# Optimization experiments

Measured on AMD Instinct MI355X. Metric: run time of the kernel, lower is better.

The kernel has to match this reference:

```python
import jax, jax.numpy as jnp
import numpy as np

D_MODEL = 64; D_INNER = 64; D_STATE = 8; DT_RANK = 4; D_CONV = 4
B, C, H, W = 16, 1024, 32, 32


def _silu(x):
    return x * jax.nn.sigmoid(x)


def _layernorm(x, g, b, eps=1e-5):
    m = x.mean(-1, keepdims=True)
    v = ((x - m) ** 2).mean(-1, keepdims=True)
    return (x - m) * jax.lax.rsqrt(v + eps) * g + b


def _rmsnorm(x, w, eps=1e-5):
    return x * jax.lax.rsqrt((x * x).mean(-1, keepdims=True) + eps) * w


def _causal_conv1d(x, w, b):
    # x: [B, D, L]; depthwise causal conv, kernel w: [D, K]
    D = x.shape[1]; K = w.shape[1]
    xp = jnp.pad(x, ((0, 0), (0, 0), (K - 1, 0)))
    y = jax.lax.conv_general_dilated(xp, w[:, None, :], (1,), 'VALID',
                                     dimension_numbers=('NCH', 'OIH', 'NCH'),
                                     feature_group_count=D)
    return y + b[None, :, None]


def _selective_scan(x, z, A_log, Dvec, xproj_w, dt_w, dt_b):
    # x, z: [B, D, L]
    A = -jnp.exp(A_log)                                    # [D, N]
    xdb = jnp.einsum('bdl,kd->blk', x, xproj_w)            # [B, L, R+2N]
    dt_lr = xdb[..., :DT_RANK]
    Bc = xdb[..., DT_RANK:DT_RANK + D_STATE]               # [B, L, N]
    Cc = xdb[..., DT_RANK + D_STATE:]                      # [B, L, N]
    dt = jax.nn.softplus(jnp.einsum('blr,dr->bld', dt_lr, dt_w) + dt_b)  # [B, L, D]
    dA = jnp.exp(dt[..., None] * A[None, None])            # [B, L, D, N]
    dBx = dt[..., None] * Bc[:, :, None, :] * x.transpose(0, 2, 1)[..., None]  # [B, L, D, N]

    def step(h, inp):
        dA_t, dBx_t, C_t = inp
        h = dA_t * h + dBx_t                               # [B, D, N]
        return h, jnp.einsum('bdn,bn->bd', h, C_t)

    h0 = jnp.zeros((x.shape[0], x.shape[1], D_STATE), x.dtype)
    _, ys = jax.lax.scan(step, h0, (dA.transpose(1, 0, 2, 3),
                                    dBx.transpose(1, 0, 2, 3),
                                    Cc.transpose(1, 0, 2)))
    y = ys.transpose(1, 2, 0) + Dvec[None, :, None] * x    # [B, D, L]
    return y * _silu(z)


def _mamba_branch(u, in_w, conv_w, conv_b, xproj_w, dt_w, dt_b, A_log, Dvec):
    # u: [B, L, d_model]
    xz = jnp.einsum('bld,ed->bel', u, in_w)                # [B, 2*D_INNER, L]
    x, z = jnp.split(xz, 2, axis=1)
    x = _silu(_causal_conv1d(x, conv_w, conv_b))
    return _selective_scan(x, z, A_log, Dvec, xproj_w, dt_w, dt_b)


def setup_inputs():
    key = jax.random.key(0)
    ks = jax.random.split(key, 20)
    rn = lambda i, shape, s=1.0: jax.random.normal(ks[i], shape, dtype=jnp.float32) * s
    s4d = jnp.log(jnp.tile(jnp.arange(1, D_STATE + 1, dtype=jnp.float32)[None, :], (D_INNER, 1)))
    return {
        'img1': rn(0, (B, C, H, W)),
        'img2': rn(1, (B, C, H, W)),
        'pre_w': rn(2, (D_MODEL, 1), 0.3),
        'pre_b': rn(3, (D_MODEL,), 0.1),
        'ln_g': jnp.ones((D_MODEL,), jnp.float32),
        'ln_b': jnp.zeros((D_MODEL,), jnp.float32),
        'in_w': rn(4, (2 * D_INNER, D_MODEL), 0.1),
        'in_b_w': rn(5, (2 * D_INNER, D_MODEL), 0.1),
        'conv_w': rn(6, (D_INNER, D_CONV), 0.3),
        'conv_bias': rn(7, (D_INNER,), 0.1),
        'convb_w': rn(8, (D_INNER, D_CONV), 0.3),
        'convb_bias': rn(9, (D_INNER,), 0.1),
        'xproj_w': rn(10, (DT_RANK + 2 * D_STATE, D_INNER), 0.1),
        'xprojb_w': rn(11, (DT_RANK + 2 * D_STATE, D_INNER), 0.1),
        'dt_w': rn(12, (D_INNER, DT_RANK), 0.1),
        'dt_bias': rn(13, (D_INNER,), 0.1),
        'dtb_w': rn(14, (D_INNER, DT_RANK), 0.1),
        'dtb_bias': rn(15, (D_INNER,), 0.1),
        'A_log': s4d,
        'A_b_log': s4d,
        'Dp': jnp.ones((D_INNER,), jnp.float32),
        'Dp_b': jnp.ones((D_INNER,), jnp.float32),
        'norm_w': jnp.ones((D_INNER,), jnp.float32),
        'out_w': rn(16, (D_MODEL, D_INNER), 0.1),
        'post_w': rn(17, (1, D_MODEL), 0.3),
        'post_b': jnp.zeros((1,), jnp.float32),
    }


def reference(img1, img2, pre_w, pre_b, ln_g, ln_b, in_w, in_b_w, conv_w, conv_bias,
              convb_w, convb_bias, xproj_w, xprojb_w, dt_w, dt_bias, dtb_w, dtb_bias,
              A_log, A_b_log, Dp, Dp_b, norm_w, out_w, post_w, post_b):
    # AdaptiveMaxPool2d((1,1)) + squeeze(-1) -> [B, C, 1]
    p1 = jnp.max(img1, axis=(2, 3))[..., None]
    p2 = jnp.max(img2, axis=(2, 3))[..., None]
    # pre_linear: Linear(1, 64) then LayerNorm(64)  -> [B, C(=L), 64]
    x1 = _layernorm(p1 * pre_w[:, 0] + pre_b, ln_g, ln_b)
    x2 = _layernorm(p2 * pre_w[:, 0] + pre_b, ln_g, ln_b)
    # bimamba v3 (cross): forward scan on x1, reversed scan on extra_emb=x2
    out_f = _mamba_branch(x1, in_w, conv_w, conv_bias, xproj_w, dt_w, dt_bias, A_log, Dp)
    out_b = _mamba_branch(x2[:, ::-1, :], in_b_w, convb_w, convb_bias, xprojb_w,
                          dtb_w, dtb_bias, A_b_log, Dp_b)[:, :, ::-1]
    y = (out_f + out_b).transpose(0, 2, 1)                 # [B, L, D_INNER]
    y = _rmsnorm(y, norm_w)                                # use_norm=True
    y = jnp.einsum('bld,ed->ble', y, out_w)                # out_proj (no bias)
    att = jnp.einsum('bld,od->blo', y, post_w) + post_b    # post_linear -> [B, C, 1]
    return jax.nn.sigmoid(att[..., None])                  # [B, C, 1, 1]
```

## Files before the change

### kernel.cpp

```cpp
#include <hip/hip_runtime.h>
#include <math.h>

typedef float    f32x4 __attribute__((ext_vector_type(4)));
typedef _Float16 f16x4 __attribute__((ext_vector_type(4)));

#define NCH 32
#define CLN 32

#define OFF_P     0
#define OFF_Q     524288
#define OFF_HIN   1048576
#define OFF_AN    1572864
#define OFF_WZ    1638400
#define OFF_VEW   1638784
#define OFF_AL2   1638848
#define OFF_TILEH 1640448
#define DTT_H 0
#define SXT_H 2097152
#define BCT_H 4194304

#define LOG2E 1.4426950408889634f
#define LN2   0.6931471805599453f

__device__ __forceinline__ float fexp2(float x){ return __builtin_amdgcn_exp2f(x); }
__device__ __forceinline__ float flog2(float x){ return __builtin_amdgcn_logf(x); }
__device__ __forceinline__ float frcp (float x){ return __builtin_amdgcn_rcpf(x); }
__device__ __forceinline__ float fsigmoid(float x){ return frcp(1.f + fexp2(-x*LOG2E)); }
__device__ __forceinline__ float fsilu(float x){ return x * fsigmoid(x); }
__device__ __forceinline__ float fsoftplus(float x){
  return fmaxf(x, 0.f) + LN2 * flog2(1.f + fexp2(-fabsf(x)*LOG2E));
}

__device__ __forceinline__ float wave_rsum(float v){
  #pragma unroll
  for (int o = 1; o < 64; o <<= 1) v += __shfl_xor(v, o, 64);
  return v;
}
__device__ __forceinline__ float wave_rmax(float v){
  #pragma unroll
  for (int o = 1; o < 64; o <<= 1) v = fmaxf(v, __shfl_xor(v, o, 64));
  return v;
}

struct Smem {
  float a1[36], a2[36], a3[36];
  float xpt[20*65];
  float dtlr[32*4];
  float sxt[64*37];
  float dtt[32*64];
  float bct[32*16];
  float gw[64], gb[64], lnbs[64];
  float W[384];
  float cst[4];
};

__device__ __forceinline__ void consts_ln(float* gw, float* gb, float* lnbs, float* cst, int t,
    const float* pre_w, const float* pre_b, const float* ln_g, const float* ln_b){
  if (t < 64){
    float w = pre_w[t], b = pre_b[t];
    float mw = wave_rsum(w) * (1.f/64.f);
    float mb = wave_rsum(b) * (1.f/64.f);
    float wc = w - mw, bc = b - mb;
    float Av = wave_rsum(wc*wc) * (1.f/64.f);
    float Bq = wave_rsum(wc*bc) * (1.f/64.f);
    float Cq = wave_rsum(bc*bc) * (1.f/64.f);
    gw[t] = wc * ln_g[t];
    gb[t] = bc * ln_g[t];
    lnbs[t] = ln_b[t];
    if (t == 0){ cst[0] = Av; cst[1] = Bq; cst[2] = Cq; }
  }
}

__device__ __forceinline__ void proj_body(
    Smem& S, int t,
    const float* __restrict__ cw, const float* __restrict__ cb,
    const float* __restrict__ xpw, const float* __restrict__ dw,
    const float* __restrict__ dbv){
  for (int i = t; i < 20*64; i += 512){
    int k = i >> 6, d = i & 63;
    S.xpt[k*65 + d] = xpw[i];
  }
  __syncthreads();
  {
    int d = t & 63, lq = t >> 6;
    float cw0=cw[d*4], cw1=cw[d*4+1], cw2=cw[d*4+2], cw3=cw[d*4+3];
    float cbd = cb[d];
    float W1d = S.W[d], W2d = S.W[128+d], W3d = S.W[256+d];
    #pragma unroll
    for (int j = 0; j < 4; ++j){
      int ll = lq*4 + j;
      float A1 = cw0*S.a1[ll] + cw1*S.a1[ll+1] + cw2*S.a1[ll+2] + cw3*S.a1[ll+3];
      float A2 = cw0*S.a2[ll] + cw1*S.a2[ll+1] + cw2*S.a2[ll+2] + cw3*S.a2[ll+3];
      float A3 = cw0*S.a3[ll] + cw1*S.a3[ll+1] + cw2*S.a3[ll+2] + cw3*S.a3[ll+3];
      float xc = W1d*A1 + W2d*A2 + W3d*A3 + cbd;
      S.sxt[d*37 + ll] = fsilu(xc);
    }
  }
  __syncthreads();
  {
    int ll = t >> 4, k = t & 15;
    float acc = 0.f;
    #pragma unroll 8
    for (int d = 0; d < 64; ++d) acc += S.xpt[(4+k)*65 + d] * S.sxt[d*37 + ll];
    S.bct[ll*16 + k] = acc;
  }
  if (t < 128){
    int ll = t >> 2, r = t & 3;
    float acc = 0.f;
    #pragma unroll 8
    for (int d = 0; d < 64; ++d) acc += S.xpt[r*65 + d] * S.sxt[d*37 + ll];
    S.dtlr[ll*4 + r] = acc;
  }
  __syncthreads();
  {
    int d = t & 63, lq = t >> 6;
    float w0=dw[d*4], w1=dw[d*4+1], w2=dw[d*4+2], w3=dw[d*4+3];
    float bd = dbv[d];
    #pragma unroll
    for (int j = 0; j < 4; ++j){
      int ll = lq*4 + j;
      float raw = bd + w0*S.dtlr[ll*4] + w1*S.dtlr[ll*4+1]
                     + w2*S.dtlr[ll*4+2] + w3*S.dtlr[ll*4+3];
      S.dtt[ll*64 + d] = fsoftplus(raw);
    }
  }
  __syncthreads();
}

__global__ void __launch_bounds__(512) k_projA(
    const float* __restrict__ img1, const float* __restrict__ img2,
    const float* pre_w, const float* pre_b, const float* ln_g, const float* ln_b,
    const float* in_w, const float* in_b_w, const float* A_log, const float* A_b_log,
    const float* conv_w, const float* conv_b, const float* convb_w, const float* convb_b,
    const float* xproj_w, const float* xprojb_w,
    const float* dt_w, const float* dt_b, const float* dtb_w, const float* dtb_b,
    const float* norm_w, const float* out_w, const float* post_w,
    float* __restrict__ ws){
  __shared__ __align__(16) Smem S;
  int bi = blockIdx.x;
  int c = bi & 31, bq = bi >> 5, br = bq >> 4, b = bq & 15;
  int t = threadIdx.x;
  int wv = t >> 6, lane = t & 63;
  const float* img = br ? img2 : img1;
  #pragma unroll
  for (int k = 0; k < 5; ++k){
    int i = wv + k*8;
    if (i < 35){
      bool valid = (c > 0) || (i >= 3);
      if (valid){
        int l = br ? (1026 - c*32 - i) : (c*32 - 3 + i);
        const f32x4* rp = (const f32x4*)(img + ((size_t)(b*1024 + l))*1024) + lane;
        f32x4 q0 = __builtin_nontemporal_load(rp +   0);
        f32x4 q1 = __builtin_nontemporal_load(rp +  64);
        f32x4 q2 = __builtin_nontemporal_load(rp + 128);
        f32x4 q3 = __builtin_nontemporal_load(rp + 192);
        float m = fmaxf(fmaxf(fmaxf(q0.x,q0.y), fmaxf(q0.z,q0.w)),
                        fmaxf(fmaxf(q1.x,q1.y), fmaxf(q1.z,q1.w)));
        m = fmaxf(m, fmaxf(fmaxf(fmaxf(q2.x,q2.y), fmaxf(q2.z,q2.w)),
                           fmaxf(fmaxf(q3.x,q3.y), fmaxf(q3.z,q3.w))));
        m = wave_rmax(m);
        if (lane == 0) S.a1[i] = m;
      } else if (lane == 0) S.a1[i] = 0.f;
    }
  }
  consts_ln(S.gw, S.gb, S.lnbs, S.cst, t, pre_w, pre_b, ln_g, ln_b);
  __syncthreads();
  if (t < 128){
    const float* iw = br ? in_b_w : in_w;
    float s1 = 0.f, s2 = 0.f, s3 = 0.f;
    #pragma unroll 8
    for (int d = 0; d < 64; ++d){
      float w = iw[t*64 + d];
      s1 += w * S.gw[d]; s2 += w * S.gb[d]; s3 += w * S.lnbs[d];
    }
    S.W[      t] = s1;
    S.W[128 + t] = s2;
    S.W[256 + t] = s3;
  }
  float A2r = -fexp2((br ? A_b_log : A_log)[t] * LOG2E) * LOG2E;
  __syncthreads();
  if (t < 36){
    bool ok = (t < 35) && ((c > 0) || (t >= 3));
    float m = ok ? S.a1[t] : 0.f;
    float Av = S.cst[0], Bq = S.cst[1], Cq = S.cst[2];
    float inv = rsqrtf(m*m*Av + 2.f*m*Bq + Cq + 1e-5f);
    S.a1[t] = ok ? m*inv : 0.f;
    S.a2[t] = ok ? inv   : 0.f;
    S.a3[t] = ok ? 1.f   : 0.f;
  }
  proj_body(S, t,
            br ? convb_w : conv_w,  br ? convb_b : conv_b,
            br ? xprojb_w : xproj_w, br ? dtb_w : dt_w, br ? dtb_b : dt_b);
  {
    _Float16* th = (_Float16*)(ws + OFF_TILEH);
    int dd = t >> 3, tt0 = (t & 7)*4;
    f32x4 sv; sv.x = S.sxt[dd*37+tt0];   sv.y = S.sxt[dd*37+tt0+1];
              sv.z = S.sxt[dd*37+tt0+2]; sv.w = S.sxt[dd*37+tt0+3];
    *(f16x4*)(th + SXT_H + (size_t)bi*2048 + dd*32 + tt0) =
        __builtin_convertvector(sv, f16x4);
    f32x4 dv; dv.x = S.dtt[t*4];   dv.y = S.dtt[t*4+1];
              dv.z = S.dtt[t*4+2]; dv.w = S.dtt[t*4+3];
    *(f16x4*)(th + DTT_H + (size_t)bi*2048 + t*4) =
        __builtin_convertvector(dv, f16x4);
    if (t < 128){
      f32x4 bv; bv.x = S.bct[t*4];   bv.y = S.bct[t*4+1];
                bv.z = S.bct[t*4+2]; bv.w = S.bct[t*4+3];
      *(f16x4*)(th + BCT_H + (size_t)bi*512 + t*4) =
          __builtin_convertvector(bv, f16x4);
    }
    if (t < 32){
      ws[OFF_AN + (size_t)bi*64 + t]      = S.a1[t+3];
      ws[OFF_AN + (size_t)bi*64 + 32 + t] = S.a2[t+3];
    }
  }
  if (bi == 0 || bi == 512){
    ws[OFF_AL2 + br*512 + t] = A2r;
    if (t < 64){
      ws[OFF_WZ + br*192 +       t] = S.W[64 + t];
      ws[OFF_WZ + br*192 +  64 + t] = S.W[128 + 64 + t];
      ws[OFF_WZ + br*192 + 128 + t] = S.W[256 + 64 + t];
    }
    if (bi == 0 && t < 64){
      float s = 0.f;
      #pragma unroll 8
      for (int e = 0; e < 64; ++e) s += post_w[e] * out_w[e*64 + t];
      ws[OFF_VEW + t] = s * norm_w[t];
    }
  }
  int d = wv*8 + (lane >> 3), n = lane & 7;
  float P = 1.f, Q = 0.f;
  #pragma unroll 4
  for (int tt = 0; tt < CLN; ++tt){
    float dtv = S.dtt[tt*64 + d];
    float xv  = S.sxt[d*37 + tt];
    float bv  = S.bct[tt*16 + n];
    float da  = fexp2(dtv * A2r);
    Q = fmaf(da, Q, dtv * bv * xv);
    P *= da;
  }
  ws[OFF_P + (size_t)bi*512 + t] = P;
  ws[OFF_Q + (size_t)bi*512 + t] = Q;
}

__global__ void __launch_bounds__(256) k_scanB(float* __restrict__ ws){
  int gid = blockIdx.x*256 + threadIdx.x;
  int bq = gid >> 9, dn = gid & 511;
  size_t base = (size_t)bq*NCH*512 + dn;
  float P[NCH], Q[NCH];
  #pragma unroll
  for (int c = 0; c < NCH; ++c){
    P[c] = ws[OFF_P + base + (size_t)c*512];
    Q[c] = ws[OFF_Q + base + (size_t)c*512];
  }
  float h = 0.f;
  #pragma unroll
  for (int c = 0; c < NCH; ++c){
    ws[OFF_HIN + base + (size_t)c*512] = h;
    h = fmaf(P[c], h, Q[c]);
  }
}

__global__ void __launch_bounds__(1024) k_scanY(
    const float* Dp, const float* Dp_b, const float* post_b,
    const float* __restrict__ ws, float* __restrict__ out){
  __shared__ __align__(16) struct {
    float dtt[2][2048];
    float sxt[2][2368];
    float bct[2][512];
    float an[2][64];
    float ylds[2][CLN*65];
  } C;
  int bi = blockIdx.x;
  int oc = bi & 31, b = bi >> 5;
  int t = threadIdx.x;
  int team = t >> 9, u = t & 511;
  int lane = t & 63;
  int wv_all = t >> 6;
  int d = ((u >> 6) << 3) + ((u & 63) >> 3), n = u & 7;
  int ti = team ? ((b+16)*32 + (31 - oc)) : (b*32 + oc);
  const _Float16* th = (const _Float16*)(ws + OFF_TILEH);
  f16x4 dvh = *(const f16x4*)(th + DTT_H + (size_t)ti*2048 + u*4);
  f16x4 svh = *(const f16x4*)(th + SXT_H + (size_t)ti*2048 + u*4);
  float h   = ws[OFF_HIN + (size_t)ti*512 + u];
  float A2r = ws[OFF_AL2 + team*512 + u];
  float W1z = ws[OFF_WZ + team*192 +       d];
  float W2z = ws[OFF_WZ + team*192 +  64 + d];
  float W3z = ws[OFF_WZ + team*192 + 128 + d];
  float Dpd = (team ? Dp_b : Dp)[d];
  float ve  = ws[OFF_VEW + lane];
  float pb  = post_b[0];
  f16x4 bvh;
  f32x4 av4;
  if (u < 128) bvh = *(const f16x4*)(th + BCT_H + (size_t)ti*512 + u*4);
  if (u < 16)  av4 = *(const f32x4*)(ws + OFF_AN + (size_t)ti*64 + u*4);
  {
    f32x4 dv = __builtin_convertvector(dvh, f32x4);
    f32x4 sv = __builtin_convertvector(svh, f32x4);
    *(f32x4*)&C.dtt[team][u*4] = dv;
    int dd = u >> 3, tt0 = (u & 7)*4;
    C.sxt[team][dd*37+tt0+0] = sv.x; C.sxt[team][dd*37+tt0+1] = sv.y;
    C.sxt[team][dd*37+tt0+2] = sv.z; C.sxt[team][dd*37+tt0+3] = sv.w;
    if (u < 128){
      f32x4 bv = __builtin_convertvector(bvh, f32x4);
      *(f32x4*)&C.bct[team][u*4] = bv;
    }
    if (u < 16)  *(f32x4*)&C.an[team][u*4]  = av4;
  }
  __syncthreads();
  {
    const float* dtt = C.dtt[team];
    const float* sxt = C.sxt[team];
    const float* bct = C.bct[team];
    const float* an  = C.an[team];
    float* yl = C.ylds[team];
    #pragma unroll 4
    for (int tt = 0; tt < CLN; ++tt){
      float dtv = dtt[tt*64 + d];
      float xv  = sxt[d*37 + tt];
      float bv  = bct[tt*16 + n];
      float cv  = bct[tt*16 + 8 + n];
      float da  = fexp2(dtv * A2r);
      h = fmaf(da, h, dtv * bv * xv);
      float pv = h * cv;
      pv += __shfl_xor(pv, 1, 64);
      pv += __shfl_xor(pv, 2, 64);
      pv += __shfl_xor(pv, 4, 64);
      if (n == 0){
        float y = pv + Dpd * xv;
        float zv = an[tt]*W1z + an[32+tt]*W2z + W3z;
        float g = fsilu(zv);
        int row = team ? (31 - tt) : tt;
        yl[row*65 + d] = y * g;
      }
    }
  }
  __syncthreads();
  #pragma unroll
  for (int j = 0; j < 2; ++j){
    int row = wv_all*2 + j;
    float v = C.ylds[0][row*65 + lane] + C.ylds[1][row*65 + lane];
    float ss = v*v, dp = v*ve;
    #pragma unroll
    for (int o = 1; o < 64; o <<= 1){
      ss += __shfl_xor(ss, o, 64);
      dp += __shfl_xor(dp, o, 64);
    }
    if (lane == 0){
      float rstd = rsqrtf(ss*(1.f/64.f) + 1e-5f);
      out[b*1024 + oc*32 + row] = fsigmoid(dp*rstd + pb);
    }
  }
}

extern "C" void kernel_launch(void* const* d_in, const int* in_sizes, int n_in,
                              void* d_out, int out_size, void* d_ws, size_t ws_size,
                              hipStream_t stream){
  const float* img1      = (const float*)d_in[0];
  const float* img2      = (const float*)d_in[1];
  const float* pre_w     = (const float*)d_in[2];
  const float* pre_b     = (const float*)d_in[3];
  const float* ln_g      = (const float*)d_in[4];
  const float* ln_b      = (const float*)d_in[5];
  const float* in_w      = (const float*)d_in[6];
  const float* in_b_w    = (const float*)d_in[7];
  const float* conv_w    = (const float*)d_in[8];
  const float* conv_bias = (const float*)d_in[9];
  const float* convb_w   = (const float*)d_in[10];
  const float* convb_bias= (const float*)d_in[11];
  const float* xproj_w   = (const float*)d_in[12];
  const float* xprojb_w  = (const float*)d_in[13];
  const float* dt_w      = (const float*)d_in[14];
  const float* dt_bias   = (const float*)d_in[15];
  const float* dtb_w     = (const float*)d_in[16];
  const float* dtb_bias  = (const float*)d_in[17];
  const float* A_log     = (const float*)d_in[18];
  const float* A_b_log   = (const float*)d_in[19];
  const float* Dp        = (const float*)d_in[20];
  const float* Dp_b      = (const float*)d_in[21];
  const float* norm_w    = (const float*)d_in[22];
  const float* out_w     = (const float*)d_in[23];
  const float* post_w    = (const float*)d_in[24];
  const float* post_b    = (const float*)d_in[25];
  float* ws  = (float*)d_ws;
  float* out = (float*)d_out;

  k_projA<<<1024, 512, 0, stream>>>(img1, img2, pre_w, pre_b, ln_g, ln_b,
                                    in_w, in_b_w, A_log, A_b_log,
                                    conv_w, conv_bias, convb_w, convb_bias,
                                    xproj_w, xprojb_w, dt_w, dt_bias, dtb_w, dtb_bias,
                                    norm_w, out_w, post_w, ws);
  k_scanB<<<64, 256, 0, stream>>>(ws);
  k_scanY<<<512, 1024, 0, stream>>>(Dp, Dp_b, post_b, ws, out);
}
```

Baseline: 68.88 us.

## Give each scanY thread four SSM states and shrink blocks to 256 threads

k_scanY now runs 256 threads per block, with each thread owning four of the eight state entries for one channel. This replaces one state per thread, cuts the shuffle reduction to a single xor step, and vectorises the h/A loads. The dt tile is stored transposed (d-major, padded to 36) in both kernels, and the scan keeps fp16 tiles in LDS, converting them in registers to save LDS and conversion passes. The trade-off is less thread-level parallelism per block and four serial exp2 calls per step per thread, in exchange for lower shuffle and LDS overhead.

```diff
diff --git a/kernel.cpp b/kernel.cpp
--- a/kernel.cpp
+++ b/kernel.cpp
@@ -47,7 +47,7 @@
   float xpt[20*65];
   float dtlr[32*4];
   float sxt[64*37];
-  float dtt[32*64];
+  float dtt[64*36];
   float bct[32*16];
   float gw[64], gb[64], lnbs[64];
   float W[384];
@@ -121,7 +121,7 @@
       int ll = lq*4 + j;
       float raw = bd + w0*S.dtlr[ll*4] + w1*S.dtlr[ll*4+1]
                      + w2*S.dtlr[ll*4+2] + w3*S.dtlr[ll*4+3];
-      S.dtt[ll*64 + d] = fsoftplus(raw);
+      S.dtt[d*36 + ll] = fsoftplus(raw);
     }
   }
   __syncthreads();
@@ -198,9 +198,8 @@
               sv.z = S.sxt[dd*37+tt0+2]; sv.w = S.sxt[dd*37+tt0+3];
     *(f16x4*)(th + SXT_H + (size_t)bi*2048 + dd*32 + tt0) =
         __builtin_convertvector(sv, f16x4);
-    f32x4 dv; dv.x = S.dtt[t*4];   dv.y = S.dtt[t*4+1];
-              dv.z = S.dtt[t*4+2]; dv.w = S.dtt[t*4+3];
-    *(f16x4*)(th + DTT_H + (size_t)bi*2048 + t*4) =
+    f32x4 dv = *(const f32x4*)&S.dtt[dd*36 + tt0];
+    *(f16x4*)(th + DTT_H + (size_t)bi*2048 + dd*32 + tt0) =
         __builtin_convertvector(dv, f16x4);
     if (t < 128){
       f32x4 bv; bv.x = S.bct[t*4];   bv.y = S.bct[t*4+1];
@@ -231,7 +230,7 @@
   float P = 1.f, Q = 0.f;
   #pragma unroll 4
   for (int tt = 0; tt < CLN; ++tt){
-    float dtv = S.dtt[tt*64 + d];
+    float dtv = S.dtt[d*36 + tt];
     float xv  = S.sxt[d*37 + tt];
     float bv  = S.bct[tt*16 + n];
     float da  = fexp2(dtv * A2r);
@@ -260,84 +259,80 @@
   }
 }
 
-__global__ void __launch_bounds__(1024) k_scanY(
+__global__ void __launch_bounds__(256) k_scanY(
     const float* Dp, const float* Dp_b, const float* post_b,
     const float* __restrict__ ws, float* __restrict__ out){
   __shared__ __align__(16) struct {
-    float dtt[2][2048];
-    float sxt[2][2368];
-    float bct[2][512];
-    float an[2][64];
-    float ylds[2][CLN*65];
+    _Float16 dth[2][64*36];
+    _Float16 sxh[2][64*36];
+    _Float16 bch[2][512];
+    float    an [2][64];
+    float    ylds[2][CLN*65];
   } C;
   int bi = blockIdx.x;
   int oc = bi & 31, b = bi >> 5;
   int t = threadIdx.x;
-  int team = t >> 9, u = t & 511;
+  int team = t >> 7, u = t & 127;
   int lane = t & 63;
-  int wv_all = t >> 6;
-  int d = ((u >> 6) << 3) + ((u & 63) >> 3), n = u & 7;
+  int d = u >> 1, np = u & 1;
   int ti = team ? ((b+16)*32 + (31 - oc)) : (b*32 + oc);
   const _Float16* th = (const _Float16*)(ws + OFF_TILEH);
-  f16x4 dvh = *(const f16x4*)(th + DTT_H + (size_t)ti*2048 + u*4);
-  f16x4 svh = *(const f16x4*)(th + SXT_H + (size_t)ti*2048 + u*4);
-  float h   = ws[OFF_HIN + (size_t)ti*512 + u];
-  float A2r = ws[OFF_AL2 + team*512 + u];
+  f32x4 hv  = *(const f32x4*)(ws + OFF_HIN + (size_t)ti*512 + u*4);
+  f32x4 a2v = *(const f32x4*)(ws + OFF_AL2 + team*512 + u*4);
   float W1z = ws[OFF_WZ + team*192 +       d];
   float W2z = ws[OFF_WZ + team*192 +  64 + d];
   float W3z = ws[OFF_WZ + team*192 + 128 + d];
   float Dpd = (team ? Dp_b : Dp)[d];
   float ve  = ws[OFF_VEW + lane];
   float pb  = post_b[0];
-  f16x4 bvh;
-  f32x4 av4;
-  if (u < 128) bvh = *(const f16x4*)(th + BCT_H + (size_t)ti*512 + u*4);
-  if (u < 16)  av4 = *(const f32x4*)(ws + OFF_AN + (size_t)ti*64 + u*4);
-  {
-    f32x4 dv = __builtin_convertvector(dvh, f32x4);
-    f32x4 sv = __builtin_convertvector(svh, f32x4);
-    *(f32x4*)&C.dtt[team][u*4] = dv;
-    int dd = u >> 3, tt0 = (u & 7)*4;
-    C.sxt[team][dd*37+tt0+0] = sv.x; C.sxt[team][dd*37+tt0+1] = sv.y;
-    C.sxt[team][dd*37+tt0+2] = sv.z; C.sxt[team][dd*37+tt0+3] = sv.w;
-    if (u < 128){
-      f32x4 bv = __builtin_convertvector(bvh, f32x4);
-      *(f32x4*)&C.bct[team][u*4] = bv;
-    }
-    if (u < 16)  *(f32x4*)&C.an[team][u*4]  = av4;
-  }
-  __syncthreads();
-  {
-    const float* dtt = C.dtt[team];
-    const float* sxt = C.sxt[team];
-    const float* bct = C.bct[team];
-    const float* an  = C.an[team];
-    float* yl = C.ylds[team];
-    #pragma unroll 4
+  #pragma unroll
+  for (int k = 0; k < 4; ++k){
+    int g = u + k*128;
+    int dd = g >> 3, tt0 = (g & 7)*4;
+    f16x4 dh = *(const f16x4*)(th + DTT_H + (size_t)ti*2048 + g*4);
+    f16x4 sh = *(const f16x4*)(th + SXT_H + (size_t)ti*2048 + g*4);
+    *(f16x4*)&C.dth[team][dd*36 + tt0] = dh;
+    *(f16x4*)&C.sxh[team][dd*36 + tt0] = sh;
+  }
+  *(f16x4*)&C.bch[team][u*4] = *(const f16x4*)(th + BCT_H + (size_t)ti*512 + u*4);
+  if (u < 16) *(f32x4*)&C.an[team][u*4] = *(const f32x4*)(ws + OFF_AN + (size_t)ti*64 + u*4);
+  __syncthreads();
+  {
+    float h0 = hv.x, h1 = hv.y, h2 = hv.z, h3 = hv.w;
+    f32x4 dt4, sx4;
+    #pragma unroll
     for (int tt = 0; tt < CLN; ++tt){
-      float dtv = dtt[tt*64 + d];
-      float xv  = sxt[d*37 + tt];
-      float bv  = bct[tt*16 + n];
-      float cv  = bct[tt*16 + 8 + n];
-      float da  = fexp2(dtv * A2r);
-      h = fmaf(da, h, dtv * bv * xv);
-      float pv = h * cv;
+      if ((tt & 3) == 0){
+        dt4 = __builtin_convertvector(*(const f16x4*)&C.dth[team][d*36 + tt], f32x4);
+        sx4 = __builtin_convertvector(*(const f16x4*)&C.sxh[team][d*36 + tt], f32x4);
+      }
+      float dtv = dt4[tt & 3];
+      float xv  = sx4[tt & 3];
+      f32x4 bf = __builtin_convertvector(
+          *(const f16x4*)&C.bch[team][tt*16 + np*4], f32x4);
+      f32x4 cf = __builtin_convertvector(
+          *(const f16x4*)&C.bch[team][tt*16 + 8 + np*4], f32x4);
+      float dx = dtv * xv;
+      h0 = fmaf(fexp2(dtv * a2v.x), h0, dx * bf.x);
+      h1 = fmaf(fexp2(dtv * a2v.y), h1, dx * bf.y);
+      h2 = fmaf(fexp2(dtv * a2v.z), h2, dx * bf.z);
+      h3 = fmaf(fexp2(dtv * a2v.w), h3, dx * bf.w);
+      float pv = fmaf(h0, cf.x, fmaf(h1, cf.y, fmaf(h2, cf.z, h3 * cf.w)));
       pv += __shfl_xor(pv, 1, 64);
-      pv += __shfl_xor(pv, 2, 64);
-      pv += __shfl_xor(pv, 4, 64);
-      if (n == 0){
+      if (np == 0){
         float y = pv + Dpd * xv;
-        float zv = an[tt]*W1z + an[32+tt]*W2z + W3z;
+        float zv = C.an[team][tt]*W1z + C.an[team][32+tt]*W2z + W3z;
         float g = fsilu(zv);
         int row = team ? (31 - tt) : tt;
-        yl[row*65 + d] = y * g;
+        C.ylds[team][row*65 + d] = y * g;
       }
     }
   }
   __syncthreads();
-  #pragma unroll
-  for (int j = 0; j < 2; ++j){
-    int row = wv_all*2 + j;
+  int wv4 = t >> 6;
+  #pragma unroll
+  for (int j = 0; j < 8; ++j){
+    int row = wv4*8 + j;
     float v = C.ylds[0][row*65 + lane] + C.ylds[1][row*65 + lane];
     float ss = v*v, dp = v*ve;
     #pragma unroll
@@ -390,5 +385,5 @@
                                     xproj_w, xprojb_w, dt_w, dt_bias, dtb_w, dtb_bias,
                                     norm_w, out_w, post_w, ws);
   k_scanB<<<64, 256, 0, stream>>>(ws);
-  k_scanY<<<512, 1024, 0, stream>>>(Dp, Dp_b, post_b, ws, out);
-}
+  k_scanY<<<512, 256, 0, stream>>>(Dp, Dp_b, post_b, ws, out);
+}
```

Result: faster. 58.93 us (-14.4%).
